# Performance work log

Measured on AMD Instinct MI355X. Metric: run time of the kernel, lower is better.

Reference implementation:

```python
import jax, jax.numpy as jnp
import numpy as np

MARGIN = 0.5
N_CLASSES = 100

def setup_inputs() -> dict:
    key = jax.random.key(0)
    k1, k2 = jax.random.split(key)
    n, d = 8192, 128
    inputs = jax.random.normal(k1, (n, d), dtype=jnp.float32)
    targets = jax.random.randint(k2, (n,), 0, N_CLASSES, dtype=jnp.int64)
    return {"inputs": inputs, "targets": targets}

def reference(inputs, targets):
    # pairwise squared euclidean distances: [n, n]
    sq = jnp.sum(inputs * inputs, axis=1)  # [n]
    dist = sq[:, None] + sq[None, :] - 2.0 * (inputs @ inputs.T)
    dist = jnp.maximum(dist, 0.0)
    # positive mask: same label (diagonal included, matching original)
    mask = targets[:, None] == targets[None, :]  # [n, n] bool
    big = jnp.float32(1e30)
    dist_ap = jnp.max(jnp.where(mask, dist, -big), axis=1)  # hardest positive per row
    dist_an = jnp.min(jnp.where(mask, big, dist), axis=1)   # hardest negative per row
    loss = jnp.sum(jax.nn.relu(dist_ap - dist_an + MARGIN))
    return loss
```

## Files before the change

kernel.cpp:

```cpp
#include <hip/hip_runtime.h>
#include <hip/hip_bf16.h>

#define D 128
#define MARGIN 0.5f
#define NSPLIT 16

typedef __attribute__((ext_vector_type(8))) short bf16x8;
typedef __attribute__((ext_vector_type(4))) float f32x4;

__global__ void prep_kernel(const float* __restrict__ x,
                            float* __restrict__ sq,
                            unsigned* __restrict__ ap,
                            unsigned* __restrict__ an,
                            __hip_bfloat16* __restrict__ xb,
                            float* __restrict__ out, int n) {
    int tid = threadIdx.x;
    int row = blockIdx.x * 4 + (tid >> 6);
    int lane = tid & 63;
    const float2* xr = (const float2*)(x + (size_t)row * D);
    float2 v = xr[lane];
    __hip_bfloat162 b2;
    b2.x = __float2bfloat16(v.x);
    b2.y = __float2bfloat16(v.y);
    ((__hip_bfloat162*)(xb + (size_t)row * D))[lane] = b2;
    float s = v.x * v.x + v.y * v.y;
    #pragma unroll
    for (int o = 32; o > 0; o >>= 1) s += __shfl_xor(s, o, 64);
    if (lane == 0) {
        sq[row] = s;
        ap[row] = 0u;
        an[row] = 0x7F800000u;
    }
    if (blockIdx.x == 0 && tid == 0) *out = 0.0f;
}

__launch_bounds__(256, 4)
__global__ void gram_kernel(const __hip_bfloat16* __restrict__ xb,
                            const float* __restrict__ sq,
                            const int* __restrict__ tgt,
                            unsigned* __restrict__ ap,
                            unsigned* __restrict__ an, int n) {
    __shared__ __align__(16) __hip_bfloat16 Bs[2][64 * D];

    const int tid  = threadIdx.x;
    const int wid  = tid >> 6;
    const int lane = tid & 63;
    const int quad = lane >> 4;
    const int l    = lane & 15;
    const int i0   = blockIdx.x * 128;
    const int jspan = n / NSPLIT;
    const int njit  = jspan / 64;
    const int j0    = blockIdx.y * jspan;
    const int rowbase = i0 + wid * 32;

    bf16x8 afrag[2][4];
    {
        const __hip_bfloat16* abase = xb + (size_t)(rowbase + l) * D + quad * 8;
        #pragma unroll
        for (int mt = 0; mt < 2; ++mt)
            #pragma unroll
            for (int ks = 0; ks < 4; ++ks)
                afrag[mt][ks] = *(const bf16x8*)(abase + (size_t)mt * 16 * D + ks * 32);
    }

    int li[2][4];
    #pragma unroll
    for (int mt = 0; mt < 2; ++mt)
        #pragma unroll
        for (int reg = 0; reg < 4; ++reg)
            li[mt][reg] = tgt[rowbase + mt * 16 + quad * 4 + reg];

    float lap[8], lan[8];
    #pragma unroll
    for (int k = 0; k < 8; ++k) { lap[k] = -1e30f; lan[k] = 1e30f; }

    const int q0 = wid * 256;
    const char* xbb = (const char*)xb;

    #define PREFETCH(jt0, buf)                                                \
        do {                                                                  \
            _Pragma("unroll")                                                 \
            for (int i_ = 0; i_ < 4; ++i_) {                                  \
                int q_ = q0 + i_ * 64 + lane;                                 \
                int r_ = q_ >> 4;                                             \
                int c_ = (q_ & 15) ^ (r_ & 15);                               \
                const char* g_ = xbb + (size_t)((jt0) + r_) * 256             \
                                     + (size_t)c_ * 16;                       \
                char* l_ = (char*)&Bs[buf][0] + (size_t)(q0 + i_ * 64) * 16;  \
                __builtin_amdgcn_global_load_lds(                             \
                    (const __attribute__((address_space(1))) void*)g_,        \
                    (__attribute__((address_space(3))) void*)l_, 16, 0, 0);   \
            }                                                                 \
        } while (0)

    PREFETCH(j0, 0);
    __syncthreads();

    for (int jj = 0; jj < njit; ++jj) {
        const int cur = jj & 1;
        if (jj < njit - 1) PREFETCH(j0 + (jj + 1) * 64, cur ^ 1);

        const char* Bb = (const char*)&Bs[cur][0];
        const int jbase = j0 + jj * 64;
        #pragma unroll
        for (int jt = 0; jt < 4; ++jt) {
            f32x4 acc0 = (f32x4){0.f, 0.f, 0.f, 0.f};
            f32x4 acc1 = (f32x4){0.f, 0.f, 0.f, 0.f};
            #pragma unroll
            for (int ks = 0; ks < 4; ++ks) {
                int q = (jt * 16 + l) * 16 + ((ks * 4 + quad) ^ l);
                bf16x8 bfr = *(const bf16x8*)(Bb + (size_t)q * 16);
                acc0 = __builtin_amdgcn_mfma_f32_16x16x32_bf16(afrag[0][ks], bfr, acc0, 0, 0, 0);
                acc1 = __builtin_amdgcn_mfma_f32_16x16x32_bf16(afrag[1][ks], bfr, acc1, 0, 0, 0);
            }
            float sjc = sq[jbase + jt * 16 + l];
            int   tjc = tgt[jbase + jt * 16 + l];
            #pragma unroll
            for (int reg = 0; reg < 4; ++reg) {
                float t0 = fmaf(-2.0f, acc0[reg], sjc);
                float t1 = fmaf(-2.0f, acc1[reg], sjc);
                bool s0 = (li[0][reg] == tjc);
                bool s1 = (li[1][reg] == tjc);
                lap[reg]     = fmaxf(lap[reg],     s0 ? t0 : -1e30f);
                lan[reg]     = fminf(lan[reg],     s0 ? 1e30f : t0);
                lap[4 + reg] = fmaxf(lap[4 + reg], s1 ? t1 : -1e30f);
                lan[4 + reg] = fminf(lan[4 + reg], s1 ? 1e30f : t1);
            }
        }

        __syncthreads();
    }
    #undef PREFETCH

    #pragma unroll
    for (int mt = 0; mt < 2; ++mt)
        #pragma unroll
        for (int reg = 0; reg < 4; ++reg) {
            float p = lap[mt * 4 + reg], q = lan[mt * 4 + reg];
            #pragma unroll
            for (int o = 1; o < 16; o <<= 1) {
                p = fmaxf(p, __shfl_xor(p, o, 64));
                q = fminf(q, __shfl_xor(q, o, 64));
            }
            if (l == mt * 4 + reg) {
                int gi = rowbase + mt * 16 + quad * 4 + reg;
                float s = sq[gi];
                atomicMax(&ap[gi], __float_as_uint(fmaxf(s + p, 0.0f)));
                atomicMin(&an[gi], __float_as_uint(fmaxf(s + q, 0.0f)));
            }
        }
}

__global__ void final_kernel(const unsigned* __restrict__ ap,
                             const unsigned* __restrict__ an,
                             float* __restrict__ out, int n) {
    int i = blockIdx.x * blockDim.x + threadIdx.x;
    float v = 0.f;
    if (i < n) {
        float p = __uint_as_float(ap[i]);
        float q = __uint_as_float(an[i]);
        v = fmaxf(p - q + MARGIN, 0.0f);
    }
    #pragma unroll
    for (int o = 32; o > 0; o >>= 1) v += __shfl_xor(v, o, 64);
    __shared__ float ws[4];
    int lane = threadIdx.x & 63, w = threadIdx.x >> 6;
    if (lane == 0) ws[w] = v;
    __syncthreads();
    if (threadIdx.x == 0) atomicAdd(out, ws[0] + ws[1] + ws[2] + ws[3]);
}

extern "C" void kernel_launch(void* const* d_in, const int* in_sizes, int n_in,
                              void* d_out, int out_size, void* d_ws, size_t ws_size,
                              hipStream_t stream) {
    const float* x   = (const float*)d_in[0];
    const int*   tgt = (const int*)d_in[1];
    float* out = (float*)d_out;
    const int n = in_sizes[1];

    float*          sq = (float*)d_ws;
    unsigned*       ap = (unsigned*)((char*)d_ws + (size_t)n * 4);
    unsigned*       an = ap + n;
    __hip_bfloat16* xb = (__hip_bfloat16*)((char*)d_ws + (size_t)n * 12);

    prep_kernel<<<n / 4, 256, 0, stream>>>(x, sq, ap, an, xb, out, n);
    dim3 grid(n / 128, NSPLIT);
    gram_kernel<<<grid, 256, 0, stream>>>(xb, sq, tgt, ap, an, n);
    final_kernel<<<n / 256, 256, 0, stream>>>(ap, an, out, n);
}
```

Measured before the change: 90.55 us.

## Sort rows by class label to skip mask logic on pure-negative tiles

Adds a counting sort of rows by target label (histogram, serial scan, atomic scatter) and packs the bf16 matrix in sorted order. Each gram block then computes the label range its rows span, and for column tiles outside that range it skips the label compare and positive-max, updating only the negative min. This cuts the per-element epilogue ALU work for most tiles, at the cost of four extra small kernel launches, a serial single-thread scan, and an indirect gather in packing. The loss is a sum over rows, so permuting rows does not change the result.

```diff
diff --git a/kernel.cpp b/kernel.cpp
--- a/kernel.cpp
+++ b/kernel.cpp
@@ -4,20 +4,60 @@
 #define D 128
 #define MARGIN 0.5f
 #define NSPLIT 16
+#define NC 100
 
 typedef __attribute__((ext_vector_type(8))) short bf16x8;
 typedef __attribute__((ext_vector_type(4))) float f32x4;
 
-__global__ void prep_kernel(const float* __restrict__ x,
+__global__ void zero_kernel(int* __restrict__ hist, float* __restrict__ out) {
+    if (threadIdx.x < NC) hist[threadIdx.x] = 0;
+    if (threadIdx.x == 0) *out = 0.0f;
+}
+
+__global__ void hist_kernel(const int* __restrict__ tgt, int* __restrict__ hist, int n) {
+    int i = blockIdx.x * blockDim.x + threadIdx.x;
+    if (i < n) atomicAdd(&hist[tgt[i]], 1);
+}
+
+__global__ void scan_kernel(const int* __restrict__ hist,
+                            int* __restrict__ starts,
+                            int* __restrict__ ends,
+                            int* __restrict__ cursor) {
+    if (threadIdx.x == 0) {
+        int acc = 0;
+        for (int c = 0; c < NC; ++c) {
+            starts[c] = acc;
+            cursor[c] = acc;
+            acc += hist[c];
+            ends[c] = acc;
+        }
+    }
+}
+
+__global__ void scatter_kernel(const int* __restrict__ tgt,
+                               int* __restrict__ cursor,
+                               int* __restrict__ perm,
+                               int* __restrict__ stgt, int n) {
+    int i = blockIdx.x * blockDim.x + threadIdx.x;
+    if (i < n) {
+        int c = tgt[i];
+        int p = atomicAdd(&cursor[c], 1);
+        perm[p] = i;
+        stgt[p] = c;
+    }
+}
+
+__global__ void pack_kernel(const float* __restrict__ x,
+                            const int* __restrict__ perm,
                             float* __restrict__ sq,
                             unsigned* __restrict__ ap,
                             unsigned* __restrict__ an,
-                            __hip_bfloat16* __restrict__ xb,
-                            float* __restrict__ out, int n) {
+                            __hip_bfloat16* __restrict__ xb, int n) {
     int tid = threadIdx.x;
     int row = blockIdx.x * 4 + (tid >> 6);
     int lane = tid & 63;
-    const float2* xr = (const float2*)(x + (size_t)row * D);
+    int orig = perm[row];
+    const float2* xr = (const float2*)(x + (size_t)orig * D);
     float2 v = xr[lane];
     __hip_bfloat162 b2;
     b2.x = __float2bfloat16(v.x);
@@ -31,13 +71,14 @@
         ap[row] = 0u;
         an[row] = 0x7F800000u;
     }
-    if (blockIdx.x == 0 && tid == 0) *out = 0.0f;
 }
 
 __launch_bounds__(256, 4)
 __global__ void gram_kernel(const __hip_bfloat16* __restrict__ xb,
                             const float* __restrict__ sq,
-                            const int* __restrict__ tgt,
+                            const int* __restrict__ stgt,
+                            const int* __restrict__ starts,
+                            const int* __restrict__ ends,
                             unsigned* __restrict__ ap,
                             unsigned* __restrict__ an, int n) {
     __shared__ __align__(16) __hip_bfloat16 Bs[2][64 * D];
@@ -53,6 +94,9 @@
     const int j0    = blockIdx.y * jspan;
     const int rowbase = i0 + wid * 32;
 
+    const int u0 = starts[stgt[i0]];
+    const int u1 = ends[stgt[i0 + 127]];
+
     bf16x8 afrag[2][4];
     {
         const __hip_bfloat16* abase = xb + (size_t)(rowbase + l) * D + quad * 8;
@@ -68,7 +112,7 @@
     for (int mt = 0; mt < 2; ++mt)
         #pragma unroll
         for (int reg = 0; reg < 4; ++reg)
-            li[mt][reg] = tgt[rowbase + mt * 16 + quad * 4 + reg];
+            li[mt][reg] = stgt[rowbase + mt * 16 + quad * 4 + reg];
 
     float lap[8], lan[8];
     #pragma unroll
@@ -102,6 +146,8 @@
 
         const char* Bb = (const char*)&Bs[cur][0];
         const int jbase = j0 + jj * 64;
+        const bool mixed = (jbase < u1) && (jbase + 64 > u0);
+
         #pragma unroll
         for (int jt = 0; jt < 4; ++jt) {
             f32x4 acc0 = (f32x4){0.f, 0.f, 0.f, 0.f};
@@ -114,20 +160,29 @@
                 acc1 = __builtin_amdgcn_mfma_f32_16x16x32_bf16(afrag[1][ks], bfr, acc1, 0, 0, 0);
             }
             float sjc = sq[jbase + jt * 16 + l];
-            int   tjc = tgt[jbase + jt * 16 + l];
-            #pragma unroll
-            for (int reg = 0; reg < 4; ++reg) {
-                float t0 = fmaf(-2.0f, acc0[reg], sjc);
-                float t1 = fmaf(-2.0f, acc1[reg], sjc);
-                bool s0 = (li[0][reg] == tjc);
-                bool s1 = (li[1][reg] == tjc);
-                lap[reg]     = fmaxf(lap[reg],     s0 ? t0 : -1e30f);
-                lan[reg]     = fminf(lan[reg],     s0 ? 1e30f : t0);
-                lap[4 + reg] = fmaxf(lap[4 + reg], s1 ? t1 : -1e30f);
-                lan[4 + reg] = fminf(lan[4 + reg], s1 ? 1e30f : t1);
+            if (mixed) {
+                int tjc = stgt[jbase + jt * 16 + l];
+                #pragma unroll
+                for (int reg = 0; reg < 4; ++reg) {
+                    float t0 = fmaf(-2.0f, acc0[reg], sjc);
+                    float t1 = fmaf(-2.0f, acc1[reg], sjc);
+                    bool s0 = (li[0][reg] == tjc);
+                    bool s1 = (li[1][reg] == tjc);
+                    lap[reg]     = fmaxf(lap[reg],     s0 ? t0 : -1e30f);
+                    lan[reg]     = fminf(lan[reg],     s0 ? 1e30f : t0);
+                    lap[4 + reg] = fmaxf(lap[4 + reg], s1 ? t1 : -1e30f);
+                    lan[4 + reg] = fminf(lan[4 + reg], s1 ? 1e30f : t1);
+                }
+            } else {
+                #pragma unroll
+                for (int reg = 0; reg < 4; ++reg) {
+                    float t0 = fmaf(-2.0f, acc0[reg], sjc);
+                    float t1 = fmaf(-2.0f, acc1[reg], sjc);
+                    lan[reg]     = fminf(lan[reg],     t0);
+                    lan[4 + reg] = fminf(lan[4 + reg], t1);
+                }
             }
         }
-
         __syncthreads();
     }
     #undef PREFETCH
@@ -178,13 +233,24 @@
     float* out = (float*)d_out;
     const int n = in_sizes[1];
 
-    float*          sq = (float*)d_ws;
-    unsigned*       ap = (unsigned*)((char*)d_ws + (size_t)n * 4);
-    unsigned*       an = ap + n;
-    __hip_bfloat16* xb = (__hip_bfloat16*)((char*)d_ws + (size_t)n * 12);
-
-    prep_kernel<<<n / 4, 256, 0, stream>>>(x, sq, ap, an, xb, out, n);
+    char* w = (char*)d_ws;
+    float*          sq     = (float*)w;                  w += (size_t)n * 4;
+    unsigned*       ap     = (unsigned*)w;               w += (size_t)n * 4;
+    unsigned*       an     = (unsigned*)w;               w += (size_t)n * 4;
+    int*            perm   = (int*)w;                    w += (size_t)n * 4;
+    int*            stgt   = (int*)w;                    w += (size_t)n * 4;
+    int*            hist   = (int*)w;                    w += 256 * 4;
+    int*            starts = (int*)w;                    w += 256 * 4;
+    int*            ends   = (int*)w;                    w += 256 * 4;
+    int*            cursor = (int*)w;                    w += 256 * 4;
+    __hip_bfloat16* xb     = (__hip_bfloat16*)w;
+
+    zero_kernel<<<1, 256, 0, stream>>>(hist, out);
+    hist_kernel<<<n / 256, 256, 0, stream>>>(tgt, hist, n);
+    scan_kernel<<<1, 64, 0, stream>>>(hist, starts, ends, cursor);
+    scatter_kernel<<<n / 256, 256, 0, stream>>>(tgt, cursor, perm, stgt, n);
+    pack_kernel<<<n / 4, 256, 0, stream>>>(x, perm, sq, ap, an, xb, n);
     dim3 grid(n / 128, NSPLIT);
-    gram_kernel<<<grid, 256, 0, stream>>>(xb, sq, tgt, ap, an, n);
+    gram_kernel<<<grid, 256, 0, stream>>>(xb, sq, stgt, starts, ends, ap, an, n);
     final_kernel<<<n / 256, 256, 0, stream>>>(ap, an, out, n);
 }
```

Result: slower. 114.2 us (+26.1%).

## Fuse final reduction into gram kernel via last-block counter and retune split

Applied to the files above, without the earlier changes.

Removes the separate final reduction kernel: each gram block increments a global done counter, and the last block to finish sums the per-row hinge terms and writes the output directly. NSPLIT goes from 16 to 20, with tile ranges computed by integer division so spans need not divide evenly, and launch bounds rise to 5 blocks per CU. This saves one kernel launch and changes grid size and occupancy. In exchange a single block runs a serial 8192-element reduction at the tail, and every block now pays an extra fence and atomic.

```diff
diff --git a/kernel.cpp b/kernel.cpp
--- a/kernel.cpp
+++ b/kernel.cpp
@@ -3,7 +3,7 @@
 
 #define D 128
 #define MARGIN 0.5f
-#define NSPLIT 16
+#define NSPLIT 20
 
 typedef __attribute__((ext_vector_type(8))) short bf16x8;
 typedef __attribute__((ext_vector_type(4))) float f32x4;
@@ -13,7 +13,7 @@
                             unsigned* __restrict__ ap,
                             unsigned* __restrict__ an,
                             __hip_bfloat16* __restrict__ xb,
-                            float* __restrict__ out, int n) {
+                            unsigned* __restrict__ done, int n) {
     int tid = threadIdx.x;
     int row = blockIdx.x * 4 + (tid >> 6);
     int lane = tid & 63;
@@ -31,15 +31,17 @@
         ap[row] = 0u;
         an[row] = 0x7F800000u;
     }
-    if (blockIdx.x == 0 && tid == 0) *out = 0.0f;
+    if (blockIdx.x == 0 && tid == 0) *done = 0u;
 }
 
-__launch_bounds__(256, 4)
+__launch_bounds__(256, 5)
 __global__ void gram_kernel(const __hip_bfloat16* __restrict__ xb,
                             const float* __restrict__ sq,
                             const int* __restrict__ tgt,
                             unsigned* __restrict__ ap,
-                            unsigned* __restrict__ an, int n) {
+                            unsigned* __restrict__ an,
+                            unsigned* __restrict__ done,
+                            float* __restrict__ out, int n) {
     __shared__ __align__(16) __hip_bfloat16 Bs[2][64 * D];
 
     const int tid  = threadIdx.x;
@@ -48,9 +50,9 @@
     const int quad = lane >> 4;
     const int l    = lane & 15;
     const int i0   = blockIdx.x * 128;
-    const int jspan = n / NSPLIT;
-    const int njit  = jspan / 64;
-    const int j0    = blockIdx.y * jspan;
+    const int NT   = n / 64;
+    const int jt_begin = (blockIdx.y * NT) / NSPLIT;
+    const int jt_end   = ((blockIdx.y + 1) * NT) / NSPLIT;
     const int rowbase = i0 + wid * 32;
 
     bf16x8 afrag[2][4];
@@ -93,15 +95,15 @@
             }                                                                 \
         } while (0)
 
-    PREFETCH(j0, 0);
-    __syncthreads();
-
-    for (int jj = 0; jj < njit; ++jj) {
-        const int cur = jj & 1;
-        if (jj < njit - 1) PREFETCH(j0 + (jj + 1) * 64, cur ^ 1);
+    PREFETCH(jt_begin * 64, 0);
+    __syncthreads();
+
+    for (int jj = jt_begin; jj < jt_end; ++jj) {
+        const int cur = (jj - jt_begin) & 1;
+        if (jj + 1 < jt_end) PREFETCH((jj + 1) * 64, cur ^ 1);
 
         const char* Bb = (const char*)&Bs[cur][0];
-        const int jbase = j0 + jj * 64;
+        const int jbase = jj * 64;
         #pragma unroll
         for (int jt = 0; jt < 4; ++jt) {
             f32x4 acc0 = (f32x4){0.f, 0.f, 0.f, 0.f};
@@ -127,7 +129,6 @@
                 lan[4 + reg] = fminf(lan[4 + reg], s1 ? 1e30f : t1);
             }
         }
-
         __syncthreads();
     }
     #undef PREFETCH
@@ -149,25 +150,33 @@
                 atomicMin(&an[gi], __float_as_uint(fmaxf(s + q, 0.0f)));
             }
         }
-}
-
-__global__ void final_kernel(const unsigned* __restrict__ ap,
-                             const unsigned* __restrict__ an,
-                             float* __restrict__ out, int n) {
-    int i = blockIdx.x * blockDim.x + threadIdx.x;
+
+    __threadfence();
+    __syncthreads();
+    int* flag = (int*)&Bs[0][0];
+    if (tid == 0) {
+        unsigned old = __hip_atomic_fetch_add(done, 1u, __ATOMIC_ACQ_REL,
+                                              __HIP_MEMORY_SCOPE_AGENT);
+        *flag = (old == (unsigned)(64 * NSPLIT) - 1u) ? 1 : 0;
+    }
+    __syncthreads();
+    if (*flag == 0) return;
+
     float v = 0.f;
-    if (i < n) {
-        float p = __uint_as_float(ap[i]);
-        float q = __uint_as_float(an[i]);
-        v = fmaxf(p - q + MARGIN, 0.0f);
+    for (int i = tid; i < n; i += 256) {
+        unsigned pb = __hip_atomic_load(&ap[i], __ATOMIC_RELAXED,
+                                        __HIP_MEMORY_SCOPE_AGENT);
+        unsigned qb = __hip_atomic_load(&an[i], __ATOMIC_RELAXED,
+                                        __HIP_MEMORY_SCOPE_AGENT);
+        v += fmaxf(__uint_as_float(pb) - __uint_as_float(qb) + MARGIN, 0.0f);
     }
     #pragma unroll
     for (int o = 32; o > 0; o >>= 1) v += __shfl_xor(v, o, 64);
-    __shared__ float ws[4];
-    int lane = threadIdx.x & 63, w = threadIdx.x >> 6;
-    if (lane == 0) ws[w] = v;
-    __syncthreads();
-    if (threadIdx.x == 0) atomicAdd(out, ws[0] + ws[1] + ws[2] + ws[3]);
+    float* ws = (float*)&Bs[0][64];
+    __syncthreads();
+    if (lane == 0) ws[wid] = v;
+    __syncthreads();
+    if (tid == 0) *out = ws[0] + ws[1] + ws[2] + ws[3];
 }
 
 extern "C" void kernel_launch(void* const* d_in, const int* in_sizes, int n_in,
@@ -178,13 +187,14 @@
     float* out = (float*)d_out;
     const int n = in_sizes[1];
 
-    float*          sq = (float*)d_ws;
-    unsigned*       ap = (unsigned*)((char*)d_ws + (size_t)n * 4);
-    unsigned*       an = ap + n;
-    __hip_bfloat16* xb = (__hip_bfloat16*)((char*)d_ws + (size_t)n * 12);
-
-    prep_kernel<<<n / 4, 256, 0, stream>>>(x, sq, ap, an, xb, out, n);
+    char* w = (char*)d_ws;
+    float*          sq   = (float*)w;          w += (size_t)n * 4;
+    unsigned*       ap   = (unsigned*)w;       w += (size_t)n * 4;
+    unsigned*       an   = (unsigned*)w;       w += (size_t)n * 4;
+    unsigned*       done = (unsigned*)w;       w += 256;
+    __hip_bfloat16* xb   = (__hip_bfloat16*)w;
+
+    prep_kernel<<<n / 4, 256, 0, stream>>>(x, sq, ap, an, xb, done, n);
     dim3 grid(n / 128, NSPLIT);
-    gram_kernel<<<grid, 256, 0, stream>>>(xb, sq, tgt, ap, an, n);
-    final_kernel<<<n / 256, 256, 0, stream>>>(ap, an, out, n);
+    gram_kernel<<<grid, 256, 0, stream>>>(xb, sq, tgt, ap, an, done, out, n);
 }
```

Result: slower. 343.5 us (+279.4%).
